# Performance work log

Hardware: AMD Instinct MI355X
Metric: run time of the kernel (lower is better)

## Reference

```python
import jax, jax.numpy as jnp
import numpy as np

B, T, H = 8, 2048, 1024
F = 4096
E = 8
TOP_K = 2


def setup_inputs() -> dict:
    key = jax.random.key(0)
    ks = jax.random.split(key, 6)
    s_h = 1.0 / np.sqrt(H)
    s_f = 1.0 / np.sqrt(F)
    return {
        "hidden_states": jax.random.normal(ks[0], (B, T, H), dtype=jnp.float32),
        "gate_w": jax.random.uniform(ks[1], (H, E), minval=-s_h, maxval=s_h, dtype=jnp.float32),
        "w1": jax.random.uniform(ks[2], (E, H, F), minval=-s_h, maxval=s_h, dtype=jnp.float32),
        "b1": jax.random.uniform(ks[3], (E, F), minval=-s_h, maxval=s_h, dtype=jnp.float32),
        "w2": jax.random.uniform(ks[4], (E, F, H), minval=-s_f, maxval=s_f, dtype=jnp.float32),
        "b2": jax.random.uniform(ks[5], (E, H), minval=-s_f, maxval=s_f, dtype=jnp.float32),
    }


def reference(hidden_states, gate_w, w1, b1, w2, b2):
    b, t, h = hidden_states.shape
    # Sequence-level routing: mean over tokens -> gate logits
    seq_rep = hidden_states.mean(axis=1)                       # [B, H]
    router_logits = seq_rep @ gate_w                           # [B, E]
    probs = jax.nn.softmax(router_logits.astype(jnp.float32), axis=-1)
    top_w, top_i = jax.lax.top_k(probs, TOP_K)                 # [B, K]
    top_w = top_w / top_w.sum(axis=-1, keepdims=True)
    top_w = top_w.astype(hidden_states.dtype)
    # Dense combine weights [B, E] (zero for unselected experts)
    combine = jnp.zeros((b, E), dtype=hidden_states.dtype)
    combine = combine.at[jnp.arange(b)[:, None], top_i].set(top_w)
    out = jnp.zeros_like(hidden_states)
    for e in range(E):  # small fixed expert loop
        hmid = jax.nn.gelu(jnp.einsum("bth,hf->btf", hidden_states, w1[e]) + b1[e],
                           approximate=False)
        y = jnp.einsum("btf,fh->bth", hmid, w2[e]) + b2[e]
        out = out + combine[:, e][:, None, None] * y
    return out
```

## Files before the change

### kernel.cpp

```cpp
#include <hip/hip_runtime.h>
#include <hip/hip_bf16.h>
#include <math.h>

#define BB 8
#define TT 2048
#define HH 1024
#define FF 4096
#define EE 8

typedef __attribute__((ext_vector_type(8))) short sh8;
typedef __attribute__((ext_vector_type(4))) float f32x4;
typedef __attribute__((ext_vector_type(4))) float f4;

__device__ inline unsigned short f2bf(float f) {
  unsigned u = __builtin_bit_cast(unsigned, f);
  u += 0x7FFFu + ((u >> 16) & 1u);
  return (unsigned short)(u >> 16);
}

__device__ inline float erf_fast(float x) {
  float ax = fabsf(x);
  float t = 1.0f / (1.0f + 0.3275911f * ax);
  float y = t * (0.254829592f +
           t * (-0.284496736f +
           t * (1.421413741f +
           t * (-1.453152027f +
           t * 1.061405429f))));
  float e = __expf(-ax * ax);
  float r = 1.0f - y * e;
  return copysignf(r, x);
}

__device__ inline void gload_lds16(const void* g, void* l) {
  __builtin_amdgcn_global_load_lds(
      (const __attribute__((address_space(1))) unsigned int*)g,
      (__attribute__((address_space(3))) unsigned int*)l, 16, 0, 0);
}

__global__ __launch_bounds__(256) void convert_x(const float* __restrict__ X,
                                                 unsigned short* __restrict__ Xb) {
  size_t i = ((size_t)blockIdx.x * 256 + threadIdx.x) * 8;
  f4 v0 = *(const f4*)&X[i];
  f4 v1 = *(const f4*)&X[i + 4];
  sh8 o;
  o[0] = (short)f2bf(v0[0]); o[1] = (short)f2bf(v0[1]);
  o[2] = (short)f2bf(v0[2]); o[3] = (short)f2bf(v0[3]);
  o[4] = (short)f2bf(v1[0]); o[5] = (short)f2bf(v1[1]);
  o[6] = (short)f2bf(v1[2]); o[7] = (short)f2bf(v1[3]);
  *(sh8*)&Xb[i] = o;
}

__global__ __launch_bounds__(256) void mean_partial(const float* __restrict__ X,
                                                    float* __restrict__ partial) {
  int tc = blockIdx.x, b = blockIdx.y, t = threadIdx.x;
  float s0 = 0.f, s1 = 0.f, s2 = 0.f, s3 = 0.f;
  const float* base = X + (size_t)b * TT * HH + (size_t)tc * 128 * HH;
  for (int tt = 0; tt < 128; tt++) {
    const float* r = base + (size_t)tt * HH;
    s0 += r[t];
    s1 += r[t + 256];
    s2 += r[t + 512];
    s3 += r[t + 768];
  }
  float* o = partial + ((size_t)b * 16 + tc) * HH;
  o[t] = s0; o[t + 256] = s1; o[t + 512] = s2; o[t + 768] = s3;
}

__global__ __launch_bounds__(256) void gating_kernel(const float* __restrict__ partial,
                                                     const float* __restrict__ gw,
                                                     int* __restrict__ re,
                                                     float* __restrict__ rw) {
  int b = blockIdx.x, t = threadIdx.x;
  float acc[EE];
#pragma unroll
  for (int e = 0; e < EE; e++) acc[e] = 0.f;
  for (int jj = 0; jj < 4; jj++) {
    int h = t + jj * 256;
    float s = 0.f;
    for (int tc = 0; tc < 16; tc++) s += partial[((size_t)b * 16 + tc) * HH + h];
    s *= (1.0f / (float)TT);
#pragma unroll
    for (int e = 0; e < EE; e++) acc[e] += s * gw[h * EE + e];
  }
#pragma unroll
  for (int off = 32; off >= 1; off >>= 1) {
#pragma unroll
    for (int e = 0; e < EE; e++) acc[e] += __shfl_down(acc[e], off);
  }
  __shared__ float red[4][EE];
  if ((t & 63) == 0) {
#pragma unroll
    for (int e = 0; e < EE; e++) red[t >> 6][e] = acc[e];
  }
  __syncthreads();
  if (t == 0) {
    float lg[EE];
#pragma unroll
    for (int e = 0; e < EE; e++) lg[e] = red[0][e] + red[1][e] + red[2][e] + red[3][e];
    float mx = lg[0];
#pragma unroll
    for (int e = 1; e < EE; e++) mx = fmaxf(mx, lg[e]);
    float p[EE]; float s = 0.f;
#pragma unroll
    for (int e = 0; e < EE; e++) { p[e] = expf(lg[e] - mx); s += p[e]; }
#pragma unroll
    for (int e = 0; e < EE; e++) p[e] /= s;
    int i1 = 0;
#pragma unroll
    for (int e = 1; e < EE; e++) if (p[e] > p[i1]) i1 = e;
    int i2 = -1;
#pragma unroll
    for (int e = 0; e < EE; e++) {
      if (e == i1) continue;
      if (i2 < 0 || p[e] > p[i2]) i2 = e;
    }
    float den = p[i1] + p[i2];
    re[b * 2 + 0] = i1; rw[b * 2 + 0] = p[i1] / den;
    re[b * 2 + 1] = i2; rw[b * 2 + 1] = p[i2] / den;
  }
}

__global__ __launch_bounds__(256) void transposeE(const float* __restrict__ W,
                                                  unsigned short* __restrict__ Wt,
                                                  const int* __restrict__ re,
                                                  int K, int N) {
  int e = blockIdx.z;
  bool u = false;
#pragma unroll
  for (int p = 0; p < 16; p++) u = u || (re[p] == e);
  if (!u) return;

  __shared__ float tile[64][65];
  int kb = blockIdx.x, nb = blockIdx.y;
  const float* src = W + (size_t)e * K * N + (size_t)(kb * 64) * N + nb * 64;
  int t = threadIdx.x;
#pragma unroll
  for (int pass = 0; pass < 4; pass++) {
    int r = (t >> 4) + pass * 16;
    int c = (t & 15) * 4;
    *(f4*)&tile[r][c] = *(const f4*)&src[(size_t)r * N + c];
  }
  __syncthreads();
#pragma unroll
  for (int pass = 0; pass < 2; pass++) {
    int idx = (t + pass * 256) * 8;
    int nl = idx >> 6, k0 = idx & 63;
    sh8 o;
#pragma unroll
    for (int j = 0; j < 8; j++) o[j] = (short)f2bf(tile[k0 + j][nl]);
    *(sh8*)&Wt[(size_t)e * N * K + (size_t)(nb * 64 + nl) * K + kb * 64 + k0] = o;
  }
}


#define MFMA_CL(qm, qn, BREG)                                                      \
    __builtin_amdgcn_s_setprio(1);                                                 \
    _Pragma("unroll")                                                              \
    for (int m4 = 0; m4 < 4; m4++)                                                 \
      _Pragma("unroll")                                                            \
      for (int n2 = 0; n2 < 2; n2++)                                               \
        _Pragma("unroll")                                                          \
        for (int kk = 0; kk < 2; kk++)                                             \
          acc[(qm) * 4 + m4][(qn) * 2 + n2] =                                      \
              __builtin_amdgcn_mfma_f32_16x16x32_bf16(                             \
                  Aq[m4 * 2 + kk], BREG[n2 * 2 + kk],                              \
                  acc[(qm) * 4 + m4][(qn) * 2 + n2], 0, 0, 0);                     \
    __builtin_amdgcn_s_setprio(0);

#define PH_PRE                                                                     \
    __builtin_amdgcn_sched_barrier(0);                                             \
    __builtin_amdgcn_s_barrier();                                                  \
    asm volatile("s_waitcnt lgkmcnt(0)" ::: "memory");                             \
    __builtin_amdgcn_sched_barrier(0);

#define PH_POST(VM)                                                                \
    if ((VM) == 4) { asm volatile("s_waitcnt vmcnt(4)" ::: "memory"); }            \
    else if ((VM) == 1) { asm volatile("s_waitcnt vmcnt(0)" ::: "memory"); }       \
    __builtin_amdgcn_sched_barrier(0);                                             \
    __builtin_amdgcn_s_barrier();

#define PH1(buf, STMT, VM) do {                                                    \
    _Pragma("unroll")                                                              \
    for (int m4 = 0; m4 < 4; m4++) {                                               \
      Aq[m4 * 2]     = *(const sh8*)(pA0 + (buf) * 32768 + m4 * 2048);             \
      Aq[m4 * 2 + 1] = *(const sh8*)(pA1 + (buf) * 32768 + m4 * 2048);             \
    }                                                                              \
    _Pragma("unroll")                                                              \
    for (int n2 = 0; n2 < 2; n2++) {                                               \
      B0r[n2 * 2]     = *(const sh8*)(pB0 + (buf) * 32768 + n2 * 2048);            \
      B0r[n2 * 2 + 1] = *(const sh8*)(pB1 + (buf) * 32768 + n2 * 2048);            \
    }                                                                              \
    STMT; PH_PRE MFMA_CL(0, 0, B0r) PH_POST(VM) } while (0)

#define PH2(buf, STMT, VM) do {                                                    \
    _Pragma("unroll")                                                              \
    for (int n2 = 0; n2 < 2; n2++) {                                               \
      B1r[n2 * 2]     = *(const sh8*)(pB0 + (buf) * 32768 + 4096 + n2 * 2048);     \
      B1r[n2 * 2 + 1] = *(const sh8*)(pB1 + (buf) * 32768 + 4096 + n2 * 2048);     \
    }                                                                              \
    STMT; PH_PRE MFMA_CL(0, 1, B1r) PH_POST(VM) } while (0)

#define PH3(buf, STMT, VM) do {                                                    \
    _Pragma("unroll")                                                              \
    for (int m4 = 0; m4 < 4; m4++) {                                               \
      Aq[m4 * 2]     = *(const sh8*)(pA0 + (buf) * 32768 + 8192 + m4 * 2048);      \
      Aq[m4 * 2 + 1] = *(const sh8*)(pA1 + (buf) * 32768 + 8192 + m4 * 2048);      \
    }                                                                              \
    STMT; PH_PRE MFMA_CL(1, 1, B1r) PH_POST(VM) } while (0)

#define PH4(buf, STMT, VM) do {                                                    \
    STMT; PH_PRE MFMA_CL(1, 0, B0r) PH_POST(VM) } while (0)

#define STAGE_A(tau, q) do {                                                       \
    int kt_ = ((tau) < NTH) ? (tau) : (tau) - NTH;                                 \
    const unsigned short* ap_ = ((tau) < NTH) ? A0p : A1p;                         \
    int bo_ = ((tau) & 1) * 32768;                                                 \
    gload_lds16(ap_ + oA##q##0 + kt_ * 64, lds + lA + bo_ + (q) * 8192);           \
    gload_lds16(ap_ + oA##q##1 + kt_ * 64, lds + lA + bo_ + (q) * 8192 + 16384);   \
  } while (0)

#define STAGE_B(tau, q) do {                                                       \
    int kt_ = ((tau) < NTH) ? (tau) : (tau) - NTH;                                 \
    const unsigned short* bp_ = ((tau) < NTH) ? B0p : B1p;                         \
    int bo_ = ((tau) & 1) * 32768;                                                 \
    gload_lds16(bp_ + oB##q##0 + kt_ * 64, lds + lB + bo_ + (q) * 4096);           \
    gload_lds16(bp_ + oB##q##1 + kt_ * 64, lds + lB + bo_ + (q) * 4096 + 16384);   \
  } while (0)

template <int MODE>
__global__ __launch_bounds__(512, 1) void gemm8p(
    const unsigned short* __restrict__ XorH,
    const unsigned short* __restrict__ Wt,
    const float* __restrict__ bias,
    const int* __restrict__ re,
    const float* __restrict__ rw,
    unsigned short* __restrict__ hmid_out,
    float* __restrict__ out) {
  extern __shared__ char lds[];

  constexpr int NT  = (MODE == 0) ? (HH / 64) : (2 * FF / 64);
  constexpr int NTH = (MODE == 0) ? NT : (FF / 64);

  int P = blockIdx.x;
  int t = threadIdx.x;
  int lane = t & 63, wv = t >> 6;
  int wr = wv >> 2, wc = wv & 3;
  int ln = lane & 15, kq = lane >> 4;

  const unsigned short *A0p, *A1p, *B0p, *B1p;
  int lda, ldb;
  int pair = 0, b, e0, e1, mb, nb;
  if constexpr (MODE == 0) {
    pair = (P & 7) * 2 + ((P >> 3) & 1);
    int idx = P >> 4;
    mb = idx & 7; nb = idx >> 3;
    b = pair >> 1;
    e0 = re[pair]; e1 = e0;
    A0p = XorH + (size_t)b * TT * HH + (size_t)mb * 256 * HH; A1p = A0p; lda = HH;
    B0p = Wt + (size_t)e0 * FF * HH + (size_t)nb * 256 * HH; B1p = B0p; ldb = HH;
  } else {
    b = P & 7;
    int idx = P >> 3;
    nb = idx & 3; mb = idx >> 2;
    e0 = re[2 * b]; e1 = re[2 * b + 1];
    A0p = XorH + (size_t)(2 * b) * TT * FF + (size_t)mb * 256 * FF;
    A1p = A0p + (size_t)TT * FF; lda = FF;
    B0p = Wt + (size_t)e0 * FF * HH + (size_t)nb * 256 * FF;
    B1p = Wt + (size_t)e1 * FF * HH + (size_t)nb * 256 * FF; ldb = FF;
  }

  int lrow = t >> 3;
  int lrB8 = (t >> 8) * 64 + ((t >> 3) & 31);
  int clel = ((t & 7) ^ ((t >> 3) & 7)) * 8;
  size_t oA00 = (size_t)(lrow)*lda + clel;
  size_t oA01 = (size_t)(128 + lrow) * lda + clel;
  size_t oA10 = (size_t)(64 + lrow) * lda + clel;
  size_t oA11 = (size_t)(192 + lrow) * lda + clel;
  size_t oB00 = (size_t)(lrB8)*ldb + clel;
  size_t oB01 = (size_t)(128 + lrB8) * ldb + clel;
  size_t oB10 = (size_t)(32 + lrB8) * ldb + clel;
  size_t oB11 = (size_t)(160 + lrB8) * ldb + clel;
  int lA = lrow * 128 + (t & 7) * 16;
  int lB = 65536 + lrB8 * 128 + (t & 7) * 16;
  char* pA0 = lds + wr * 16384 + ln * 128 + ((kq ^ (ln & 7)) * 16);
  char* pA1 = lds + wr * 16384 + ln * 128 + (((4 + kq) ^ (ln & 7)) * 16);
  char* pB0 = lds + 65536 + wc * 8192 + ln * 128 + ((kq ^ (ln & 7)) * 16);
  char* pB1 = lds + 65536 + wc * 8192 + ln * 128 + (((4 + kq) ^ (ln & 7)) * 16);

  f32x4 acc[8][4];
#pragma unroll
  for (int m = 0; m < 8; m++)
#pragma unroll
    for (int n = 0; n < 4; n++) acc[m][n] = (f32x4){0.f, 0.f, 0.f, 0.f};

  sh8 Aq[8], B0r[4], B1r[4];

  STAGE_A(0, 0); STAGE_B(0, 0); STAGE_A(0, 1); STAGE_B(0, 1);
  STAGE_A(1, 0); STAGE_B(1, 0);
  asm volatile("s_waitcnt vmcnt(4)" ::: "memory");
  __builtin_amdgcn_sched_barrier(0);
  __builtin_amdgcn_s_barrier();

  int T = 0;
  for (; T + 2 < NT; T += 2) {
    PH1(0, { STAGE_A(T + 1, 1); }, 0);
    PH2(0, { STAGE_B(T + 1, 1); }, 0);
    PH3(0, { STAGE_A(T + 2, 0); }, 0);
    PH4(0, { STAGE_B(T + 2, 0); }, 4);
    PH1(1, { STAGE_A(T + 2, 1); }, 0);
    PH2(1, { STAGE_B(T + 2, 1); }, 0);
    PH3(1, { STAGE_A(T + 3, 0); }, 0);
    PH4(1, { STAGE_B(T + 3, 0); }, 4);
  }
  PH1(0, { STAGE_A(T + 1, 1); }, 0);
  PH2(0, { STAGE_B(T + 1, 1); }, 0);
  PH3(0, {}, 0);
  PH4(0, {}, 1);
  PH1(1, {}, 0);
  PH2(1, {}, 0);
  PH3(1, {}, 0);
  PH4(1, {}, 0);

  if constexpr (MODE == 0) {
    float wgt = rw[pair];
    unsigned short* Cout = hmid_out + (size_t)pair * TT * FF;
    float bbv[4];
#pragma unroll
    for (int nn = 0; nn < 4; nn++)
      bbv[nn] = bias[(size_t)e0 * FF + nb * 256 + wc * 64 + nn * 16 + ln];
    __syncthreads();
#pragma unroll
    for (int mm = 0; mm < 8; mm++) {
#pragma unroll
      for (int nn = 0; nn < 4; nn++) {
        int c2 = (wc * 64 + nn * 16 + ln) * 2;
#pragma unroll
        for (int j = 0; j < 4; j++) {
          int r = wr * 128 + mm * 16 + kq * 4 + j;
          float v = acc[mm][nn][j] + bbv[nn];
          float g = 0.5f * v * (1.0f + erf_fast(v * 0.70710678118654752f));
          *(unsigned short*)(lds + r * 512 + (c2 ^ (((r >> 2) & 7) << 4))) =
              f2bf(wgt * g);
        }
      }
    }
    __syncthreads();
#pragma unroll
    for (int i = 0; i < 16; i++) {
      int r = wv * 32 + i * 2 + (lane >> 5);
      int ci = lane & 31;
      sh8 v = *(const sh8*)(lds + r * 512 + ((ci ^ ((r >> 2) & 7)) << 4));
      *(sh8*)&Cout[(size_t)(mb * 256 + r) * FF + nb * 256 + ci * 8] = v;
    }
  } else {
    float w0 = rw[2 * b], w1v = rw[2 * b + 1];
#pragma unroll
    for (int nn = 0; nn < 4; nn++) {
      int col = nb * 256 + wc * 64 + nn * 16 + ln;
      float bv = w0 * bias[(size_t)e0 * HH + col] + w1v * bias[(size_t)e1 * HH + col];
#pragma unroll
      for (int mm = 0; mm < 8; mm++) {
#pragma unroll
        for (int j = 0; j < 4; j++) {
          int row = mb * 256 + wr * 128 + mm * 16 + kq * 4 + j;
          out[(size_t)b * TT * HH + (size_t)row * HH + col] = acc[mm][nn][j] + bv;
        }
      }
    }
  }
}

extern "C" void kernel_launch(void* const* d_in, const int* in_sizes, int n_in,
                              void* d_out, int out_size, void* d_ws, size_t ws_size,
                              hipStream_t stream) {
  const float* X  = (const float*)d_in[0];
  const float* gw = (const float*)d_in[1];
  const float* w1 = (const float*)d_in[2];
  const float* pb1 = (const float*)d_in[3];
  const float* w2 = (const float*)d_in[4];
  const float* pb2 = (const float*)d_in[5];
  float* out = (float*)d_out;

  char* ws = (char*)d_ws;
  int* re = (int*)ws;
  float* rw = (float*)(ws + 64);
  float* partial = (float*)(ws + 256);
  unsigned short* Xbf = (unsigned short*)(ws + 256 + 524288);
  const size_t fixed = 256 + 524288 + (size_t)BB * TT * HH * 2;

  unsigned short* w1t = (unsigned short*)(ws + fixed);
  unsigned short* w2t = (unsigned short*)(ws + fixed + (size_t)EE * HH * FF * 2);
  unsigned short* hmid = (unsigned short*)(ws + fixed + (size_t)2 * EE * HH * FF * 2);

  hipFuncSetAttribute((const void*)gemm8p<0>,
                      hipFuncAttributeMaxDynamicSharedMemorySize, 131072);
  hipFuncSetAttribute((const void*)gemm8p<1>,
                      hipFuncAttributeMaxDynamicSharedMemorySize, 131072);

  convert_x<<<8192, 256, 0, stream>>>(X, Xbf);
  mean_partial<<<dim3(16, BB), 256, 0, stream>>>(X, partial);
  gating_kernel<<<BB, 256, 0, stream>>>(partial, gw, re, rw);

  transposeE<<<dim3(HH / 64, FF / 64, EE), 256, 0, stream>>>(w1, w1t, re, HH, FF);
  transposeE<<<dim3(FF / 64, HH / 64, EE), 256, 0, stream>>>(w2, w2t, re, FF, HH);

  gemm8p<0><<<2048, 512, 131072, stream>>>(Xbf, w1t, pb1, re, rw, hmid, nullptr);
  gemm8p<1><<<256, 512, 131072, stream>>>(hmid, w2t, pb2, re, rw, nullptr, out);
}
```

Measured before the change: 683.2 us.

## Make first GEMM persistent over 8 N-tiles with fragment-order hmid layout

Fuses the bf16 conversion and mean-partial passes over X into one prep kernel. The first expert GEMM now runs 256 blocks, each looping over eight 256-wide F tiles. It writes GELU output straight from registers in an MFMA-fragment-permuted hmid layout with nontemporal stores, which removes the LDS transpose and the second grid wave. The second GEMM reads hmid through the matching permutation, and the final output also uses nontemporal stores. The prep kernel launches only 128 blocks, which may underuse the GPU for streaming X, and the 2-byte scalar stores to hmid may be less efficient than the old 16-byte vector stores.

```diff
diff --git a/kernel.cpp b/kernel.cpp
--- a/kernel.cpp
+++ b/kernel.cpp
@@ -9,6 +9,7 @@
 #define EE 8
 
 typedef __attribute__((ext_vector_type(8))) short sh8;
+typedef __attribute__((ext_vector_type(4))) short sh4;
 typedef __attribute__((ext_vector_type(4))) float f32x4;
 typedef __attribute__((ext_vector_type(4))) float f4;
 
@@ -37,33 +38,22 @@
       (__attribute__((address_space(3))) unsigned int*)l, 16, 0, 0);
 }
 
-__global__ __launch_bounds__(256) void convert_x(const float* __restrict__ X,
-                                                 unsigned short* __restrict__ Xb) {
-  size_t i = ((size_t)blockIdx.x * 256 + threadIdx.x) * 8;
-  f4 v0 = *(const f4*)&X[i];
-  f4 v1 = *(const f4*)&X[i + 4];
-  sh8 o;
-  o[0] = (short)f2bf(v0[0]); o[1] = (short)f2bf(v0[1]);
-  o[2] = (short)f2bf(v0[2]); o[3] = (short)f2bf(v0[3]);
-  o[4] = (short)f2bf(v1[0]); o[5] = (short)f2bf(v1[1]);
-  o[6] = (short)f2bf(v1[2]); o[7] = (short)f2bf(v1[3]);
-  *(sh8*)&Xb[i] = o;
-}
-
-__global__ __launch_bounds__(256) void mean_partial(const float* __restrict__ X,
-                                                    float* __restrict__ partial) {
+__global__ __launch_bounds__(256) void prep(const float* __restrict__ X,
+                                            unsigned short* __restrict__ Xb,
+                                            float* __restrict__ partial) {
   int tc = blockIdx.x, b = blockIdx.y, t = threadIdx.x;
-  float s0 = 0.f, s1 = 0.f, s2 = 0.f, s3 = 0.f;
-  const float* base = X + (size_t)b * TT * HH + (size_t)tc * 128 * HH;
-  for (int tt = 0; tt < 128; tt++) {
-    const float* r = base + (size_t)tt * HH;
-    s0 += r[t];
-    s1 += r[t + 256];
-    s2 += r[t + 512];
-    s3 += r[t + 768];
-  }
-  float* o = partial + ((size_t)b * 16 + tc) * HH;
-  o[t] = s0; o[t + 256] = s1; o[t + 512] = s2; o[t + 768] = s3;
+  const float* src = X + ((size_t)b * TT + (size_t)tc * 128) * HH;
+  unsigned short* dst = Xb + ((size_t)b * TT + (size_t)tc * 128) * HH;
+  f4 s = {0.f, 0.f, 0.f, 0.f};
+  for (int r = 0; r < 128; ++r) {
+    f4 v = *(const f4*)&src[(size_t)r * HH + t * 4];
+    s[0] += v[0]; s[1] += v[1]; s[2] += v[2]; s[3] += v[3];
+    sh4 o;
+    o[0] = (short)f2bf(v[0]); o[1] = (short)f2bf(v[1]);
+    o[2] = (short)f2bf(v[2]); o[3] = (short)f2bf(v[3]);
+    *(sh4*)&dst[(size_t)r * HH + t * 4] = o;
+  }
+  *(f4*)&partial[((size_t)b * 16 + tc) * HH + t * 4] = s;
 }
 
 __global__ __launch_bounds__(256) void gating_kernel(const float* __restrict__ partial,
@@ -212,20 +202,52 @@
     STMT; PH_PRE MFMA_CL(1, 0, B0r) PH_POST(VM) } while (0)
 
 #define STAGE_A(tau, q) do {                                                       \
-    int kt_ = ((tau) < NTH) ? (tau) : (tau) - NTH;                                 \
-    const unsigned short* ap_ = ((tau) < NTH) ? A0p : A1p;                         \
     int bo_ = ((tau) & 1) * 32768;                                                 \
-    gload_lds16(ap_ + oA##q##0 + kt_ * 64, lds + lA + bo_ + (q) * 8192);           \
-    gload_lds16(ap_ + oA##q##1 + kt_ * 64, lds + lA + bo_ + (q) * 8192 + 16384);   \
-  } while (0)
+    if constexpr (MODE == 0) {                                                     \
+      const unsigned short* ap_ = A0p + ((tau) & 15) * 64;                         \
+      gload_lds16(ap_ + oA##q##0, lds + lA + bo_ + (q) * 8192);                    \
+      gload_lds16(ap_ + oA##q##1, lds + lA + bo_ + (q) * 8192 + 16384);            \
+    } else {                                                                       \
+      int kt_ = ((tau) < NTH) ? (tau) : (tau) - NTH;                               \
+      const unsigned short* ap_ = (((tau) < NTH) ? H0p : H1p) +                    \
+                                  (kt_ >> 2) * 65536 + (kt_ & 3) * 8192;           \
+      gload_lds16(ap_ + fA##q##0, lds + lA + bo_ + (q) * 8192);                    \
+      gload_lds16(ap_ + fA##q##1, lds + lA + bo_ + (q) * 8192 + 16384);            \
+    } } while (0)
 
 #define STAGE_B(tau, q) do {                                                       \
-    int kt_ = ((tau) < NTH) ? (tau) : (tau) - NTH;                                 \
-    const unsigned short* bp_ = ((tau) < NTH) ? B0p : B1p;                         \
     int bo_ = ((tau) & 1) * 32768;                                                 \
-    gload_lds16(bp_ + oB##q##0 + kt_ * 64, lds + lB + bo_ + (q) * 4096);           \
-    gload_lds16(bp_ + oB##q##1 + kt_ * 64, lds + lB + bo_ + (q) * 4096 + 16384);   \
-  } while (0)
+    if constexpr (MODE == 0) {                                                     \
+      const unsigned short* bp_ = w1tE +                                           \
+          (size_t)(nbh8 + ((tau) >> 4)) * (256 * HH) + ((tau) & 15) * 64;          \
+      gload_lds16(bp_ + oB##q##0, lds + lB + bo_ + (q) * 4096);                    \
+      gload_lds16(bp_ + oB##q##1, lds + lB + bo_ + (q) * 4096 + 16384);            \
+    } else {                                                                       \
+      int kt_ = ((tau) < NTH) ? (tau) : (tau) - NTH;                               \
+      const unsigned short* bp_ = (((tau) < NTH) ? B0p : B1p) + kt_ * 64;          \
+      gload_lds16(bp_ + oB##q##0, lds + lB + bo_ + (q) * 4096);                    \
+      gload_lds16(bp_ + oB##q##1, lds + lB + bo_ + (q) * 4096 + 16384);            \
+    } } while (0)
+
+#define STD8(T)                                                                    \
+    PH1(0, { STAGE_A((T) + 1, 1); }, 0);                                           \
+    PH2(0, { STAGE_B((T) + 1, 1); }, 0);                                           \
+    PH3(0, { STAGE_A((T) + 2, 0); }, 0);                                           \
+    PH4(0, { STAGE_B((T) + 2, 0); }, 4);                                           \
+    PH1(1, { STAGE_A((T) + 2, 1); }, 0);                                           \
+    PH2(1, { STAGE_B((T) + 2, 1); }, 0);                                           \
+    PH3(1, { STAGE_A((T) + 3, 0); }, 0);                                           \
+    PH4(1, { STAGE_B((T) + 3, 0); }, 4);
+
+#define TAIL8(T)                                                                   \
+    PH1(0, { STAGE_A((T) + 1, 1); }, 0);                                           \
+    PH2(0, { STAGE_B((T) + 1, 1); }, 0);                                           \
+    PH3(0, {}, 0);                                                                 \
+    PH4(0, {}, 1);                                                                 \
+    PH1(1, {}, 0);                                                                 \
+    PH2(1, {}, 0);                                                                 \
+    PH3(1, {}, 0);                                                                 \
+    PH4(1, {}, 0);
 
 template <int MODE>
 __global__ __launch_bounds__(512, 1) void gemm8p(
@@ -238,7 +260,7 @@
     float* __restrict__ out) {
   extern __shared__ char lds[];
 
-  constexpr int NT  = (MODE == 0) ? (HH / 64) : (2 * FF / 64);
+  constexpr int NT  = 128;
   constexpr int NTH = (MODE == 0) ? NT : (FF / 64);
 
   int P = blockIdx.x;
@@ -247,35 +269,49 @@
   int wr = wv >> 2, wc = wv & 3;
   int ln = lane & 15, kq = lane >> 4;
 
-  const unsigned short *A0p, *A1p, *B0p, *B1p;
-  int lda, ldb;
-  int pair = 0, b, e0, e1, mb, nb;
+  const unsigned short *A0p = nullptr, *w1tE = nullptr;
+  const unsigned short *H0p = nullptr, *H1p = nullptr, *B0p = nullptr, *B1p = nullptr;
+  int pair = 0, b, e0 = 0, e1 = 0, mb, nb = 0, nbh8 = 0;
+  int ldb;
   if constexpr (MODE == 0) {
-    pair = (P & 7) * 2 + ((P >> 3) & 1);
-    int idx = P >> 4;
-    mb = idx & 7; nb = idx >> 3;
-    b = pair >> 1;
-    e0 = re[pair]; e1 = e0;
-    A0p = XorH + (size_t)b * TT * HH + (size_t)mb * 256 * HH; A1p = A0p; lda = HH;
-    B0p = Wt + (size_t)e0 * FF * HH + (size_t)nb * 256 * HH; B1p = B0p; ldb = HH;
+    b = P & 7;
+    int k = P >> 3;
+    int pairbit = k & 1;
+    mb = (k >> 1) & 7;
+    nbh8 = (k >> 4) * 8;
+    pair = b * 2 + pairbit;
+    e0 = re[pair];
+    A0p = XorH + (size_t)b * TT * HH + (size_t)mb * 256 * HH;
+    w1tE = Wt + (size_t)e0 * FF * HH;
+    ldb = HH;
   } else {
     b = P & 7;
     int idx = P >> 3;
     nb = idx & 3; mb = idx >> 2;
     e0 = re[2 * b]; e1 = re[2 * b + 1];
-    A0p = XorH + (size_t)(2 * b) * TT * FF + (size_t)mb * 256 * FF;
-    A1p = A0p + (size_t)TT * FF; lda = FF;
+    H0p = XorH + (size_t)(2 * b) * TT * FF + (size_t)mb * 16 * 65536;
+    H1p = H0p + (size_t)TT * FF;
     B0p = Wt + (size_t)e0 * FF * HH + (size_t)nb * 256 * FF;
-    B1p = Wt + (size_t)e1 * FF * HH + (size_t)nb * 256 * FF; ldb = FF;
+    B1p = Wt + (size_t)e1 * FF * HH + (size_t)nb * 256 * FF;
+    ldb = FF;
   }
 
   int lrow = t >> 3;
   int lrB8 = (t >> 8) * 64 + ((t >> 3) & 31);
   int clel = ((t & 7) ^ ((t >> 3) & 7)) * 8;
-  size_t oA00 = (size_t)(lrow)*lda + clel;
-  size_t oA01 = (size_t)(128 + lrow) * lda + clel;
-  size_t oA10 = (size_t)(64 + lrow) * lda + clel;
-  size_t oA11 = (size_t)(192 + lrow) * lda + clel;
+  size_t oA00 = (size_t)(lrow)*HH + clel;
+  size_t oA01 = (size_t)(128 + lrow) * HH + clel;
+  size_t oA10 = (size_t)(64 + lrow) * HH + clel;
+  size_t oA11 = (size_t)(192 + lrow) * HH + clel;
+  int nnl = (clel >> 4) & 3, lnl = clel & 15;
+#define FPERM(r) ((size_t)((((r) >> 7) & 1) * 32768 +                              \
+                  ((((r) >> 4) & 7) * 16 + nnl * 4 + ((r) & 3)) * 64 +             \
+                  (((r) >> 2) & 3) * 16 + lnl))
+  size_t fA00 = FPERM(lrow);
+  size_t fA01 = FPERM(128 + lrow);
+  size_t fA10 = FPERM(64 + lrow);
+  size_t fA11 = FPERM(192 + lrow);
+#undef FPERM
   size_t oB00 = (size_t)(lrB8)*ldb + clel;
   size_t oB01 = (size_t)(128 + lrB8) * ldb + clel;
   size_t oB10 = (size_t)(32 + lrB8) * ldb + clel;
@@ -301,58 +337,47 @@
   __builtin_amdgcn_sched_barrier(0);
   __builtin_amdgcn_s_barrier();
 
-  int T = 0;
-  for (; T + 2 < NT; T += 2) {
-    PH1(0, { STAGE_A(T + 1, 1); }, 0);
-    PH2(0, { STAGE_B(T + 1, 1); }, 0);
-    PH3(0, { STAGE_A(T + 2, 0); }, 0);
-    PH4(0, { STAGE_B(T + 2, 0); }, 4);
-    PH1(1, { STAGE_A(T + 2, 1); }, 0);
-    PH2(1, { STAGE_B(T + 2, 1); }, 0);
-    PH3(1, { STAGE_A(T + 3, 0); }, 0);
-    PH4(1, { STAGE_B(T + 3, 0); }, 4);
-  }
-  PH1(0, { STAGE_A(T + 1, 1); }, 0);
-  PH2(0, { STAGE_B(T + 1, 1); }, 0);
-  PH3(0, {}, 0);
-  PH4(0, {}, 1);
-  PH1(1, {}, 0);
-  PH2(1, {}, 0);
-  PH3(1, {}, 0);
-  PH4(1, {}, 0);
-
   if constexpr (MODE == 0) {
     float wgt = rw[pair];
-    unsigned short* Cout = hmid_out + (size_t)pair * TT * FF;
-    float bbv[4];
-#pragma unroll
-    for (int nn = 0; nn < 4; nn++)
-      bbv[nn] = bias[(size_t)e0 * FF + nb * 256 + wc * 64 + nn * 16 + ln];
-    __syncthreads();
-#pragma unroll
-    for (int mm = 0; mm < 8; mm++) {
-#pragma unroll
-      for (int nn = 0; nn < 4; nn++) {
-        int c2 = (wc * 64 + nn * 16 + ln) * 2;
-#pragma unroll
-        for (int j = 0; j < 4; j++) {
-          int r = wr * 128 + mm * 16 + kq * 4 + j;
-          float v = acc[mm][nn][j] + bbv[nn];
-          float g = 0.5f * v * (1.0f + erf_fast(v * 0.70710678118654752f));
-          *(unsigned short*)(lds + r * 512 + (c2 ^ (((r >> 2) & 7) << 4))) =
-              f2bf(wgt * g);
+    for (int seg = 0; seg < 8; ++seg) {
+      int nIt = (seg == 7) ? 7 : 8;
+      for (int it = 0; it < nIt; ++it) {
+        int T = seg * 16 + it * 2;
+        STD8(T);
+      }
+      if (seg == 7) { TAIL8(126); }
+      {
+        int nbs = nbh8 + seg;
+        float bbv[4];
+#pragma unroll
+        for (int nn = 0; nn < 4; nn++)
+          bbv[nn] = bias[(size_t)e0 * FF + nbs * 256 + wc * 64 + nn * 16 + ln];
+        unsigned short* Cp = hmid_out + (size_t)pair * TT * FF +
+                             (size_t)(mb * 16 + nbs) * 65536 + wv * 8192 + lane;
+#pragma unroll
+        for (int mm = 0; mm < 8; mm++) {
+#pragma unroll
+          for (int nn = 0; nn < 4; nn++) {
+#pragma unroll
+            for (int j = 0; j < 4; j++) {
+              float v = acc[mm][nn][j] + bbv[nn];
+              float g = 0.5f * v * (1.0f + erf_fast(v * 0.70710678118654752f));
+              __builtin_nontemporal_store(f2bf(wgt * g),
+                                          Cp + (mm * 16 + nn * 4 + j) * 64);
+            }
+          }
         }
+#pragma unroll
+        for (int m = 0; m < 8; m++)
+#pragma unroll
+          for (int n = 0; n < 4; n++) acc[m][n] = (f32x4){0.f, 0.f, 0.f, 0.f};
       }
     }
-    __syncthreads();
-#pragma unroll
-    for (int i = 0; i < 16; i++) {
-      int r = wv * 32 + i * 2 + (lane >> 5);
-      int ci = lane & 31;
-      sh8 v = *(const sh8*)(lds + r * 512 + ((ci ^ ((r >> 2) & 7)) << 4));
-      *(sh8*)&Cout[(size_t)(mb * 256 + r) * FF + nb * 256 + ci * 8] = v;
+  } else {
+    for (int T = 0; T + 2 < NT; T += 2) {
+      STD8(T);
     }
-  } else {
+    TAIL8(NT - 2);
     float w0 = rw[2 * b], w1v = rw[2 * b + 1];
 #pragma unroll
     for (int nn = 0; nn < 4; nn++) {
@@ -363,7 +388,8 @@
 #pragma unroll
         for (int j = 0; j < 4; j++) {
           int row = mb * 256 + wr * 128 + mm * 16 + kq * 4 + j;
-          out[(size_t)b * TT * HH + (size_t)row * HH + col] = acc[mm][nn][j] + bv;
+          __builtin_nontemporal_store(acc[mm][nn][j] + bv,
+              &out[(size_t)b * TT * HH + (size_t)row * HH + col]);
         }
       }
     }
@@ -397,13 +423,12 @@
   hipFuncSetAttribute((const void*)gemm8p<1>,
                       hipFuncAttributeMaxDynamicSharedMemorySize, 131072);
 
-  convert_x<<<8192, 256, 0, stream>>>(X, Xbf);
-  mean_partial<<<dim3(16, BB), 256, 0, stream>>>(X, partial);
+  prep<<<dim3(16, BB), 256, 0, stream>>>(X, Xbf, partial);
   gating_kernel<<<BB, 256, 0, stream>>>(partial, gw, re, rw);
 
   transposeE<<<dim3(HH / 64, FF / 64, EE), 256, 0, stream>>>(w1, w1t, re, HH, FF);
   transposeE<<<dim3(FF / 64, HH / 64, EE), 256, 0, stream>>>(w2, w2t, re, FF, HH);
 
-  gemm8p<0><<<2048, 512, 131072, stream>>>(Xbf, w1t, pb1, re, rw, hmid, nullptr);
+  gemm8p<0><<<256, 512, 131072, stream>>>(Xbf, w1t, pb1, re, rw, hmid, nullptr);
   gemm8p<1><<<256, 512, 131072, stream>>>(hmid, w2t, pb2, re, rw, nullptr, out);
 }
```

Result: faster. 641.5 us (-6.1%).
